# Optimization experiments

Hardware: AMD Instinct MI355X
Metric: run time of the kernel (lower is better)

The kernel has to match this reference:

```python
import jax, jax.numpy as jnp
import numpy as np

SEQ_LEN = 12
EMB = 64        # embedding_dim
H = 128         # dec_h_dim
MLP = 1024      # mlp_dim
Z = 32          # z_dim
ZX = MLP + Z    # 1056, width of cat([enc_h_feat, z])
B = 32768


def setup_inputs() -> dict:
    key = jax.random.key(0)
    ks = jax.random.split(key, 16)
    s = 0.05  # weight scale to keep the recurrence stable
    return {
        "last_pos": jax.random.normal(ks[0], (B, 2), jnp.float32),
        "last_pos_rel": jax.random.normal(ks[1], (B, 2), jnp.float32),
        "enc_h_feat": jax.random.normal(ks[2], (B, MLP), jnp.float32),
        "z": jax.random.normal(ks[3], (B, Z), jnp.float32),
        "seq_start_end": jnp.zeros((1, 2), jnp.int64),
        # LSTM params (PyTorch layout: gates ordered i,f,g,o along rows)
        "W_ih": jax.random.normal(ks[4], (4 * H, ZX + EMB), jnp.float32) * s,
        "W_hh": jax.random.normal(ks[5], (4 * H, H), jnp.float32) * s,
        "b_ih": jax.random.normal(ks[6], (4 * H,), jnp.float32) * s,
        "b_hh": jax.random.normal(ks[7], (4 * H,), jnp.float32) * s,
        # mlp: Linear(ZX->MLP), ReLU, Linear(MLP->H), ReLU
        "W1": jax.random.normal(ks[8], (MLP, ZX), jnp.float32) * s,
        "b1": jax.random.normal(ks[9], (MLP,), jnp.float32) * s,
        "W2": jax.random.normal(ks[10], (H, MLP), jnp.float32) * s,
        "b2": jax.random.normal(ks[11], (H,), jnp.float32) * s,
        # spatial_embedding: Linear(2 -> EMB)
        "W_sp": jax.random.normal(ks[12], (EMB, 2), jnp.float32) * s,
        "b_sp": jax.random.normal(ks[13], (EMB,), jnp.float32) * s,
        # hidden2pos: Linear(H -> 2)
        "W_hp": jax.random.normal(ks[14], (2, H), jnp.float32) * s,
        "b_hp": jax.random.normal(ks[15], (2,), jnp.float32) * s,
    }


def _decode(last_pos, last_pos_rel, enc_h_feat, z,
            W_ih, W_hh, b_ih, b_hh, W1, b1, W2, b2, W_sp, b_sp, W_hp, b_hp):
    # initial decoder input from last relative position
    dec_inp = last_pos_rel @ W_sp.T + b_sp                     # [B, EMB]
    zx = jnp.concatenate([enc_h_feat, z], axis=1)              # [B, ZX]
    h = jax.nn.relu(jax.nn.relu(zx @ W1.T + b1) @ W2.T + b2)   # [B, H]
    c = jnp.zeros_like(h)
    # zx is constant across steps: precompute its gate contribution + biases
    W_zx, W_emb = W_ih[:, :ZX], W_ih[:, ZX:]
    zx_proj = zx @ W_zx.T + b_ih + b_hh                        # [B, 4H]

    def step(carry, _):
        h, c, last_pos, dec_inp = carry
        gates = zx_proj + dec_inp @ W_emb.T + h @ W_hh.T       # [B, 4H]
        i, f, g, o = jnp.split(gates, 4, axis=1)
        c = jax.nn.sigmoid(f) * c + jax.nn.sigmoid(i) * jnp.tanh(g)
        h = jax.nn.sigmoid(o) * jnp.tanh(c)
        rel_pos = h @ W_hp.T + b_hp                            # [B, 2]
        last_pos = rel_pos + last_pos
        dec_inp = rel_pos @ W_sp.T + b_sp
        return (h, c, last_pos, dec_inp), rel_pos

    _, pred = jax.lax.scan(step, (h, c, last_pos, dec_inp), None, length=SEQ_LEN)
    return pred  # [SEQ_LEN, B, 2]


def reference(last_pos, last_pos_rel, enc_h_feat, z, seq_start_end,
              W_ih, W_hh, b_ih, b_hh, W1, b1, W2, b2, W_sp, b_sp, W_hp, b_hp):
    # seq_start_end is unused by the original forward
    return _decode(last_pos, last_pos_rel, enc_h_feat, z,
                   W_ih, W_hh, b_ih, b_hh, W1, b1, W2, b2, W_sp, b_sp, W_hp, b_hp)
```

## Files before the change

kernel.cpp:

```cpp
#include <hip/hip_runtime.h>

#define BATCH   32768
#define SEQLEN  12
#define EMB     64
#define H       128
#define MLP     1024
#define Z       32
#define ZX      1056
#define KP      1088
#define NG      512

typedef _Float16 f16x8 __attribute__((ext_vector_type(8)));
typedef float    f32x4 __attribute__((ext_vector_type(4)));

#define S_WCAT_OFF   0u
#define S_W2H_OFF    3244032u
#define S_WHHF_OFF   3506176u
#define S_WC_OFF     3637248u
#define S_BIAS2_OFF  3641344u
#define S_T1_OFF     3643392u
#define S_GP_OFF     70752256u
#define S_H0_OFF     137861120u
#define B_WCAT_OFF   0u
#define B_W2H_OFF    3342336u
#define B_WHHF_OFF   3604480u
#define B_WC_OFF     3735552u
#define B_BIAS2_OFF  3739648u
#define B_T1_OFF     3741696u
#define B_GP_OFF     70850560u
#define B_H0_OFF     137959424u
#define B_ZX16_OFF   146348032u
#define B_TOTAL      217651200ull

__device__ __forceinline__ float sigf(float x) {
    return __builtin_amdgcn_rcpf(1.0f + __expf(-x));
}
__device__ __forceinline__ float tanhfast(float x) {
    return 2.0f * __builtin_amdgcn_rcpf(1.0f + __expf(-2.0f * x)) - 1.0f;
}

__device__ __forceinline__ void gload16(const void* g, void* l) {
    __builtin_amdgcn_global_load_lds(
        (const __attribute__((address_space(1))) unsigned int*)(unsigned long long)(uintptr_t)g,
        (__attribute__((address_space(3))) unsigned int*)(unsigned int)(uintptr_t)l,
        16, 0, 0);
}

__global__ __launch_bounds__(256) void prep_kernel(
    const float* __restrict__ W_ih, const float* __restrict__ W_hh_in,
    const float* __restrict__ b_ih, const float* __restrict__ b_hh,
    const float* __restrict__ W1,   const float* __restrict__ W2,
    const float* __restrict__ W_sp, const float* __restrict__ b_sp,
    const float* __restrict__ W_hp, int cs,
    _Float16* __restrict__ wcat, _Float16* __restrict__ w2h,
    _Float16* __restrict__ whhf, float* __restrict__ wc, float* __restrict__ bias2)
{
    const int bid = blockIdx.x;
    const int tid = threadIdx.x;
    if (bid < 1536) {
        const float* src = (bid < 1024) ? (W1 + (size_t)bid * ZX)
                                        : (W_ih + (size_t)(bid - 1024) * 1120);
        _Float16* dst = wcat + (size_t)bid * cs;
        for (int k = tid; k < cs; k += 256)
            dst[k] = (k < ZX) ? (_Float16)src[k] : (_Float16)0.f;
    } else if (bid < 1664) {
        const int n = bid - 1536;
        for (int k = tid; k < MLP; k += 256)
            w2h[n * MLP + k] = (_Float16)W2[n * MLP + k];
    } else if (bid < 1920) {
        const int n = (bid - 1664) * 2 + (tid >> 7);
        const int k = tid & 127;
        float wc0 = 0.f, wc1 = 0.f;
        for (int e = 0; e < EMB; ++e) {
            const float we = W_ih[(size_t)n * 1120 + ZX + e];
            wc0 += we * W_sp[e * 2];
            wc1 += we * W_sp[e * 2 + 1];
        }
        whhf[n * H + k] = (_Float16)(W_hh_in[n * H + k] + wc0 * W_hp[k] + wc1 * W_hp[H + k]);
    } else {
        const int t = (bid - 1920) * 256 + tid;
        if (t < 1024) {
            const int n = t >> 1, j = t & 1;
            float s = 0.f;
            for (int e = 0; e < EMB; ++e)
                s += W_ih[(size_t)n * 1120 + ZX + e] * W_sp[e * 2 + j];
            wc[t] = s;
        } else if (t < 1536) {
            const int n = t - 1024;
            float s = b_ih[n] + b_hh[n];
            for (int e = 0; e < EMB; ++e)
                s += W_ih[(size_t)n * 1120 + ZX + e] * b_sp[e];
            bias2[n] = s;
        }
    }
}

__global__ __launch_bounds__(256) void zxcast_kernel(
    const float* __restrict__ enc, const float* __restrict__ zin,
    _Float16* __restrict__ zx16)
{
    const int gid = blockIdx.x * 256 + threadIdx.x;
    if (gid < 4194304) {
        const int row = gid >> 7, cw = gid & 127;
        const float4* s = (const float4*)(enc + (size_t)row * MLP + cw * 8);
        const float4 f0 = s[0], f1 = s[1];
        f16x8 v = {(_Float16)f0.x, (_Float16)f0.y, (_Float16)f0.z, (_Float16)f0.w,
                   (_Float16)f1.x, (_Float16)f1.y, (_Float16)f1.z, (_Float16)f1.w};
        *(f16x8*)(zx16 + (size_t)row * KP + cw * 8) = v;
    } else if (gid < 4325376) {
        const int g2 = gid - 4194304;
        const int row = g2 >> 2, cw = g2 & 3;
        const float4* s = (const float4*)(zin + (size_t)row * Z + cw * 8);
        const float4 f0 = s[0], f1 = s[1];
        f16x8 v = {(_Float16)f0.x, (_Float16)f0.y, (_Float16)f0.z, (_Float16)f0.w,
                   (_Float16)f1.x, (_Float16)f1.y, (_Float16)f1.z, (_Float16)f1.w};
        *(f16x8*)(zx16 + (size_t)row * KP + MLP + cw * 8) = v;
    } else {
        const int g2 = gid - 4325376;
        const int row = g2 >> 2, cw = g2 & 3;
        f16x8 v = {};
        *(f16x8*)(zx16 + (size_t)row * KP + ZX + cw * 8) = v;
    }
}

__global__ __launch_bounds__(512, 2) void gemm1_big_kernel(
    const _Float16* __restrict__ zx16, const _Float16* __restrict__ wcat,
    const float* __restrict__ bias1, const float* __restrict__ bias2g,
    _Float16* __restrict__ t1, float* __restrict__ gperm)
{
    __shared__ _Float16 s_a[2][256 * 64];
    __shared__ _Float16 s_b[2][256 * 64];

    const int tid = threadIdx.x;
    const int b   = blockIdx.x;
    const int swz = (b & 7) * 96 + (b >> 3);
    const int mt  = swz / 6, nt = swz % 6;
    const int m0  = mt * 256, n0 = nt * 256;

    const int lane = tid & 63, wv = tid >> 6;
    const int wm   = wv >> 2,  wn = wv & 3;
    const int l15  = lane & 15, q = lane >> 4;

    const int rowS = tid >> 3;
    const int chS  = (tid & 7) ^ (rowS & 7);

    const _Float16* gA = zx16 + (size_t)(m0 + rowS) * KP + chS * 8;
    const _Float16* gB = wcat + (size_t)(n0 + rowS) * KP + chS * 8;
    const size_t rstep = (size_t)64 * KP;

    const int ph0  = q ^ (l15 & 7);
    const int ph1  = (4 + q) ^ (l15 & 7);
    const int aof0 = (wm * 128 + l15) * 64 + ph0 * 8;
    const int aof1 = (wm * 128 + l15) * 64 + ph1 * 8;
    const int bof0 = (wn * 64 + l15) * 64 + ph0 * 8;
    const int bof1 = (wn * 64 + l15) * 64 + ph1 * 8;

    f32x4 acc[8][4] = {};

    {
        _Float16* dA = &s_a[0][0] + wv * 512;
        _Float16* dB = &s_b[0][0] + wv * 512;
        #pragma unroll
        for (int j = 0; j < 4; ++j) gload16(gA + j * rstep, dA + j * 4096);
        #pragma unroll
        for (int j = 0; j < 4; ++j) gload16(gB + j * rstep, dB + j * 4096);
    }

    #pragma unroll 2
    for (int kt = 0; kt < 16; ++kt) {
        const int cur = kt & 1;
        const _Float16* sA = &s_a[cur][0];
        const _Float16* sB = &s_b[cur][0];
        _Float16* dA = &s_a[cur ^ 1][0] + wv * 512;
        _Float16* dB = &s_b[cur ^ 1][0] + wv * 512;
        const _Float16* gA1 = gA + (kt + 1) * 64;
        const _Float16* gB1 = gB + (kt + 1) * 64;

        f16x8 af[4], bf[4];

        gload16(gA1,         dA);
        gload16(gA1 + rstep, dA + 4096);
        asm volatile("s_waitcnt vmcnt(2)\n\ts_barrier" ::: "memory");
        #pragma unroll
        for (int i = 0; i < 4; ++i) af[i] = *(const f16x8*)(sA + aof0 + i * 1024);
        #pragma unroll
        for (int i = 0; i < 4; ++i) bf[i] = *(const f16x8*)(sB + bof0 + i * 1024);
        __builtin_amdgcn_s_setprio(1);
        #pragma unroll
        for (int n_ = 0; n_ < 4; ++n_)
            #pragma unroll
            for (int m_ = 0; m_ < 4; ++m_)
                acc[m_][n_] = __builtin_amdgcn_mfma_f32_16x16x32_f16(af[m_], bf[n_], acc[m_][n_], 0, 0, 0);
        __builtin_amdgcn_s_setprio(0);
        asm volatile("s_barrier" ::: "memory");

        gload16(gA1 + 2 * rstep, dA + 8192);
        gload16(gA1 + 3 * rstep, dA + 12288);
        #pragma unroll
        for (int i = 0; i < 4; ++i) af[i] = *(const f16x8*)(sA + aof0 + 4096 + i * 1024);
        asm volatile("s_barrier" ::: "memory");
        __builtin_amdgcn_s_setprio(1);
        #pragma unroll
        for (int n_ = 0; n_ < 4; ++n_)
            #pragma unroll
            for (int m_ = 0; m_ < 4; ++m_)
                acc[4 + m_][n_] = __builtin_amdgcn_mfma_f32_16x16x32_f16(af[m_], bf[n_], acc[4 + m_][n_], 0, 0, 0);
        __builtin_amdgcn_s_setprio(0);
        asm volatile("s_barrier" ::: "memory");

        gload16(gB1,         dB);
        gload16(gB1 + rstep, dB + 4096);
        #pragma unroll
        for (int i = 0; i < 4; ++i) af[i] = *(const f16x8*)(sA + aof1 + i * 1024);
        #pragma unroll
        for (int i = 0; i < 4; ++i) bf[i] = *(const f16x8*)(sB + bof1 + i * 1024);
        asm volatile("s_barrier" ::: "memory");
        __builtin_amdgcn_s_setprio(1);
        #pragma unroll
        for (int n_ = 0; n_ < 4; ++n_)
            #pragma unroll
            for (int m_ = 0; m_ < 4; ++m_)
                acc[m_][n_] = __builtin_amdgcn_mfma_f32_16x16x32_f16(af[m_], bf[n_], acc[m_][n_], 0, 0, 0);
        __builtin_amdgcn_s_setprio(0);
        asm volatile("s_barrier" ::: "memory");

        gload16(gB1 + 2 * rstep, dB + 8192);
        gload16(gB1 + 3 * rstep, dB + 12288);
        #pragma unroll
        for (int i = 0; i < 4; ++i) af[i] = *(const f16x8*)(sA + aof1 + 4096 + i * 1024);
        asm volatile("s_barrier" ::: "memory");
        __builtin_amdgcn_s_setprio(1);
        #pragma unroll
        for (int n_ = 0; n_ < 4; ++n_)
            #pragma unroll
            for (int m_ = 0; m_ < 4; ++m_)
                acc[4 + m_][n_] = __builtin_amdgcn_mfma_f32_16x16x32_f16(af[m_], bf[n_], acc[4 + m_][n_], 0, 0, 0);
        __builtin_amdgcn_s_setprio(0);
        asm volatile("s_barrier" ::: "memory");
    }

    {
        const _Float16* sA = &s_a[0][0];
        const _Float16* sB = &s_b[0][0];
        asm volatile("s_waitcnt vmcnt(0)\n\ts_barrier" ::: "memory");
        f16x8 af[4], bf[4];
        #pragma unroll
        for (int i = 0; i < 4; ++i) af[i] = *(const f16x8*)(sA + aof0 + i * 1024);
        #pragma unroll
        for (int i = 0; i < 4; ++i) bf[i] = *(const f16x8*)(sB + bof0 + i * 1024);
        __builtin_amdgcn_s_setprio(1);
        #pragma unroll
        for (int n_ = 0; n_ < 4; ++n_)
            #pragma unroll
            for (int m_ = 0; m_ < 4; ++m_)
                acc[m_][n_] = __builtin_amdgcn_mfma_f32_16x16x32_f16(af[m_], bf[n_], acc[m_][n_], 0, 0, 0);
        #pragma unroll
        for (int i = 0; i < 4; ++i) af[i] = *(const f16x8*)(sA + aof0 + 4096 + i * 1024);
        #pragma unroll
        for (int n_ = 0; n_ < 4; ++n_)
            #pragma unroll
            for (int m_ = 0; m_ < 4; ++m_)
                acc[4 + m_][n_] = __builtin_amdgcn_mfma_f32_16x16x32_f16(af[m_], bf[n_], acc[4 + m_][n_], 0, 0, 0);
        #pragma unroll
        for (int i = 0; i < 4; ++i) af[i] = *(const f16x8*)(sA + aof1 + i * 1024);
        #pragma unroll
        for (int i = 0; i < 4; ++i) bf[i] = *(const f16x8*)(sB + bof1 + i * 1024);
        #pragma unroll
        for (int n_ = 0; n_ < 4; ++n_)
            #pragma unroll
            for (int m_ = 0; m_ < 4; ++m_)
                acc[m_][n_] = __builtin_amdgcn_mfma_f32_16x16x32_f16(af[m_], bf[n_], acc[m_][n_], 0, 0, 0);
        #pragma unroll
        for (int i = 0; i < 4; ++i) af[i] = *(const f16x8*)(sA + aof1 + 4096 + i * 1024);
        #pragma unroll
        for (int n_ = 0; n_ < 4; ++n_)
            #pragma unroll
            for (int m_ = 0; m_ < 4; ++m_)
                acc[4 + m_][n_] = __builtin_amdgcn_mfma_f32_16x16x32_f16(af[m_], bf[n_], acc[4 + m_][n_], 0, 0, 0);
        __builtin_amdgcn_s_setprio(0);
    }

    if (nt < 4) {
        #pragma unroll
        for (int im = 0; im < 8; ++im)
            #pragma unroll
            for (int in_ = 0; in_ < 4; ++in_) {
                const int n = n0 + wn * 64 + in_ * 16 + l15;
                const float bb = bias1[n];
                const int mbase = m0 + wm * 128 + im * 16 + q * 4;
                #pragma unroll
                for (int r = 0; r < 4; ++r) {
                    float v = acc[im][in_][r] + bb;
                    v = v > 0.f ? v : 0.f;
                    t1[(size_t)(mbase + r) * MLP + n] = (_Float16)v;
                }
            }
    } else {
        #pragma unroll
        for (int im = 0; im < 8; ++im)
            #pragma unroll
            for (int in_ = 0; in_ < 4; ++in_) {
                const int n = (n0 - 1024) + wn * 64 + in_ * 16 + l15;
                const float bb = bias2g[n];
                const int m4 = (m0 + wm * 128 + im * 16 + q * 4) >> 2;
                float4 v;
                v.x = acc[im][in_][0] + bb;
                v.y = acc[im][in_][1] + bb;
                v.z = acc[im][in_][2] + bb;
                v.w = acc[im][in_][3] + bb;
                *(float4*)(gperm + ((size_t)m4 * NG + n) * 4) = v;
            }
    }
}

__global__ __launch_bounds__(256) void gemm1_small_kernel(
    const float* __restrict__ enc, const float* __restrict__ zin,
    const _Float16* __restrict__ wcat,
    const float* __restrict__ bias1, const float* __restrict__ bias2g,
    _Float16* __restrict__ t1, float* __restrict__ gperm)
{
    __shared__ float    s_a[128 * 32];
    __shared__ _Float16 s_b[128 * 32];

    const int tid = threadIdx.x;
    const int b = blockIdx.x;
    const int x = b & 7, s = b >> 3;
    const int mt = x * 32 + s / 12;
    const int bn = s % 12;
    const int m0 = mt * 128;

    const int lane = tid & 63, wv = tid >> 6;
    const int wm = wv >> 1, wn = wv & 1;
    const int l15 = lane & 15, q = lane >> 4;

    const int rowA = tid >> 3;
    const int chA  = (tid & 7) ^ ((tid >> 3) & 7);
    const int rowB = tid >> 2;
    const int chB  = (tid & 3) ^ ((tid >> 3) & 3);

    const int ca0 = (2 * q) ^ (l15 & 7);
    const int cb  = q ^ ((l15 >> 1) & 3);

    f32x4 acc[4][4] = {};

    for (int kt = 0; kt < 33; ++kt) {
        const float* abase;
        size_t astride;
        if (kt < 32) { abase = enc + (size_t)m0 * MLP + kt * 32; astride = MLP; }
        else         { abase = zin + (size_t)m0 * Z;             astride = Z;   }

        __syncthreads();
        #pragma unroll
        for (int i = 0; i < 4; ++i)
            gload16(abase + (size_t)(i * 32 + rowA) * astride + chA * 4,
                    s_a + i * 1024 + wv * 256);
        #pragma unroll
        for (int i = 0; i < 2; ++i)
            gload16(wcat + (size_t)(bn * 128 + i * 64 + rowB) * ZX + kt * 32 + chB * 8,
                    s_b + i * 2048 + wv * 512);
        __syncthreads();

        f16x8 af[4];
        #pragma unroll
        for (int im = 0; im < 4; ++im) {
            const float* ap = s_a + (wm * 64 + im * 16 + l15) * 32;
            const float4 f0 = *(const float4*)(ap + ca0 * 4);
            const float4 f1 = *(const float4*)(ap + (ca0 ^ 1) * 4);
            af[im] = f16x8{(_Float16)f0.x, (_Float16)f0.y, (_Float16)f0.z, (_Float16)f0.w,
                           (_Float16)f1.x, (_Float16)f1.y, (_Float16)f1.z, (_Float16)f1.w};
        }
        #pragma unroll
        for (int in_ = 0; in_ < 4; ++in_) {
            const f16x8 bf = *(const f16x8*)(s_b + (wn * 64 + in_ * 16 + l15) * 32 + cb * 8);
            #pragma unroll
            for (int im = 0; im < 4; ++im)
                acc[im][in_] = __builtin_amdgcn_mfma_f32_16x16x32_f16(af[im], bf, acc[im][in_], 0, 0, 0);
        }
    }

    if (bn < 8) {
        #pragma unroll
        for (int im = 0; im < 4; ++im)
            #pragma unroll
            for (int in_ = 0; in_ < 4; ++in_) {
                const int n = bn * 128 + wn * 64 + in_ * 16 + l15;
                const float bb = bias1[n];
                #pragma unroll
                for (int r = 0; r < 4; ++r) {
                    const int m = m0 + wm * 64 + im * 16 + q * 4 + r;
                    float v = acc[im][in_][r] + bb;
                    v = v > 0.f ? v : 0.f;
                    t1[(size_t)m * MLP + n] = (_Float16)v;
                }
            }
    } else {
        #pragma unroll
        for (int im = 0; im < 4; ++im)
            #pragma unroll
            for (int in_ = 0; in_ < 4; ++in_) {
                const int n = (bn - 8) * 128 + wn * 64 + in_ * 16 + l15;
                const float bb = bias2g[n];
                const int m4 = (m0 + wm * 64 + im * 16 + q * 4) >> 2;
                float4 v;
                v.x = acc[im][in_][0] + bb;
                v.y = acc[im][in_][1] + bb;
                v.z = acc[im][in_][2] + bb;
                v.w = acc[im][in_][3] + bb;
                *(float4*)(gperm + ((size_t)m4 * NG + n) * 4) = v;
            }
    }
}

__global__ __launch_bounds__(256) void gemm2_kernel(
    const _Float16* __restrict__ t1, const _Float16* __restrict__ w2h,
    const float* __restrict__ b2, _Float16* __restrict__ h0buf)
{
    __shared__ _Float16 s_a[2][64 * 32];
    __shared__ _Float16 s_b[2][128 * 32];

    const int tid = threadIdx.x;
    const int m0  = blockIdx.x * 64;
    const int lane = tid & 63, wv = tid >> 6;
    const int l15 = lane & 15, q = lane >> 4;

    const int rowS = tid >> 2;
    const int chS  = ((tid & 3) ^ (tid >> 2) ^ (tid >> 4)) & 3;
    const int phF  = (q ^ l15 ^ (l15 >> 2)) & 3;

    const int rowB0 = rowS, rowB1 = 64 + rowS;
    const int cB0 = ((tid & 3) ^ rowB0 ^ (rowB0 >> 2)) & 3;
    const int cB1 = ((tid & 3) ^ rowB1 ^ (rowB1 >> 2)) & 3;

    const _Float16* gA  = t1  + (size_t)(m0 + rowS) * MLP + chS * 8;
    const _Float16* gB0 = w2h + (size_t)rowB0 * MLP + cB0 * 8;
    const _Float16* gB1 = w2h + (size_t)rowB1 * MLP + cB1 * 8;

    f32x4 acc[4][2] = {};

    gload16(gA,  &s_a[0][0] + wv * 512);
    gload16(gB0, &s_b[0][0] + wv * 512);
    gload16(gB1, &s_b[0][0] + 2048 + wv * 512);

    for (int kt = 0; kt < 32; ++kt) {
        const int cur = kt & 1;
        if (kt < 31) {
            const int nxt = cur ^ 1;
            gload16(gA  + (kt + 1) * 32, &s_a[nxt][0] + wv * 512);
            gload16(gB0 + (kt + 1) * 32, &s_b[nxt][0] + wv * 512);
            gload16(gB1 + (kt + 1) * 32, &s_b[nxt][0] + 2048 + wv * 512);
            asm volatile("s_waitcnt vmcnt(3)\n\ts_barrier" ::: "memory");
        } else {
            asm volatile("s_waitcnt vmcnt(0)\n\ts_barrier" ::: "memory");
        }

        f16x8 af[4];
        #pragma unroll
        for (int im = 0; im < 4; ++im)
            af[im] = *(const f16x8*)(&s_a[cur][0] + (im * 16 + l15) * 32 + phF * 8);
        #pragma unroll
        for (int in_ = 0; in_ < 2; ++in_) {
            const f16x8 bf = *(const f16x8*)(&s_b[cur][0] + (wv * 32 + in_ * 16 + l15) * 32 + phF * 8);
            #pragma unroll
            for (int im = 0; im < 4; ++im)
                acc[im][in_] = __builtin_amdgcn_mfma_f32_16x16x32_f16(af[im], bf, acc[im][in_], 0, 0, 0);
        }
        asm volatile("s_barrier" ::: "memory");
    }

    #pragma unroll
    for (int im = 0; im < 4; ++im)
        #pragma unroll
        for (int in_ = 0; in_ < 2; ++in_) {
            const int n = wv * 32 + in_ * 16 + l15;
            const float bb = b2[n];
            #pragma unroll
            for (int r = 0; r < 4; ++r) {
                const int m = m0 + im * 16 + q * 4 + r;
                float v = acc[im][in_][r] + bb;
                v = v > 0.f ? v : 0.f;
                h0buf[(size_t)m * H + n] = (_Float16)v;
            }
        }
}

__global__ __launch_bounds__(512) void recur_kernel(
    const float* __restrict__ gperm, const _Float16* __restrict__ h0buf,
    const _Float16* __restrict__ whhf, const float* __restrict__ wc,
    const float* __restrict__ whp, const float* __restrict__ bhp,
    const float* __restrict__ lpr, float* __restrict__ out)
{
    __shared__ _Float16 s_whh[512 * 136];
    __shared__ _Float16 s_h[64 * 136];
    __shared__ float    s_p[128];
    __shared__ float    s_wc[1024];
    __shared__ float    s_whp[256];
    __shared__ float    s_bhp[2];

    const int tid = threadIdx.x;
    const int m0  = blockIdx.x * 64;
    const int lane = tid & 63, w = tid >> 6;
    const int l15 = lane & 15, q = lane >> 4;

    #pragma unroll
    for (int i = 0; i < 16; ++i) {
        const int cid = tid + i * 512;
        const int row = cid >> 4, ch = cid & 15;
        *(uint4*)(s_whh + row * 136 + ch * 8) = *(const uint4*)(whhf + row * H + ch * 8);
    }
    if (tid < 256) *(float4*)(s_wc + tid * 4)  = *(const float4*)(wc + tid * 4);
    if (tid < 64)  *(float4*)(s_whp + tid * 4) = *(const float4*)(whp + tid * 4);
    if (tid < 2)   s_bhp[tid] = bhp[tid];
    if (tid < 128) s_p[tid] = lpr[(size_t)m0 * 2 + tid];
    {
        const int row = tid >> 3, ch = tid & 7;
        *(uint4*)(s_h + row * 136 + ch * 16)     = *(const uint4*)(h0buf + (size_t)(m0 + row) * H + ch * 16);
        *(uint4*)(s_h + row * 136 + ch * 16 + 8) = *(const uint4*)(h0buf + (size_t)(m0 + row) * H + ch * 16 + 8);
    }

    f32x4 gb[4][4];
    #pragma unroll
    for (int im = 0; im < 4; ++im) {
        const int m4 = (m0 >> 2) + im * 4 + q;
        #pragma unroll
        for (int g = 0; g < 4; ++g) {
            const float4 v = *(const float4*)(gperm + ((size_t)m4 * NG + g * H + w * 16 + l15) * 4);
            gb[im][g] = f32x4{v.x, v.y, v.z, v.w};
        }
    }

    f32x4 cst[4] = {};

    __syncthreads();

    {
        const int part = tid & 3;
        const int j    = (tid >> 2) & 1;
        const int row  = tid >> 3;
        float sum = 0.f;
        #pragma unroll
        for (int u = 0; u < 4; ++u) {
            const f16x8 hv = *(const f16x8*)(s_h + row * 136 + part * 32 + u * 8);
            const float4* wp = (const float4*)(s_whp + j * H + part * 32 + u * 8);
            const float4 w0 = wp[0], w1 = wp[1];
            sum += (float)hv[0] * w0.x + (float)hv[1] * w0.y + (float)hv[2] * w0.z + (float)hv[3] * w0.w
                 + (float)hv[4] * w1.x + (float)hv[5] * w1.y + (float)hv[6] * w1.z + (float)hv[7] * w1.w;
        }
        sum += __shfl_down(sum, 2, 64);
        sum += __shfl_down(sum, 1, 64);
        if (part == 0) s_p[row * 2 + j] -= sum;
    }
    __syncthreads();

    float wc0[4], wc1[4], cg[4];
    #pragma unroll
    for (int g = 0; g < 4; ++g) {
        const int n = g * H + w * 16 + l15;
        wc0[g] = s_wc[n * 2];
        wc1[g] = s_wc[n * 2 + 1];
        cg[g]  = wc0[g] * s_bhp[0] + wc1[g] * s_bhp[1];
    }
    #pragma unroll
    for (int im = 0; im < 4; ++im)
        #pragma unroll
        for (int r = 0; r < 4; ++r) {
            const int mrow = im * 16 + q * 4 + r;
            const float pa = s_p[mrow * 2], pb = s_p[mrow * 2 + 1];
            #pragma unroll
            for (int g = 0; g < 4; ++g)
                gb[im][g][r] += pa * wc0[g] + pb * wc1[g];
        }

    for (int t = 0; t < SEQLEN; ++t) {
        f32x4 acc[4][4];
        #pragma unroll
        for (int kt = 0; kt < 4; ++kt) {
            f16x8 af[4];
            #pragma unroll
            for (int im = 0; im < 4; ++im)
                af[im] = *(const f16x8*)(s_h + (im * 16 + l15) * 136 + kt * 32 + q * 8);
            #pragma unroll
            for (int g = 0; g < 4; ++g) {
                const f16x8 bf = *(const f16x8*)(s_whh + (g * H + w * 16 + l15) * 136 + kt * 32 + q * 8);
                #pragma unroll
                for (int im = 0; im < 4; ++im)
                    acc[im][g] = __builtin_amdgcn_mfma_f32_16x16x32_f16(
                        af[im], bf, (kt == 0) ? gb[im][g] : acc[im][g], 0, 0, 0);
            }
        }
        __syncthreads();

        #pragma unroll
        for (int im = 0; im < 4; ++im) {
            #pragma unroll
            for (int r = 0; r < 4; ++r) {
                const int mrow = im * 16 + q * 4 + r;
                const float cc = sigf(acc[im][1][r]) * cst[im][r]
                               + sigf(acc[im][0][r]) * tanhfast(acc[im][2][r]);
                cst[im][r] = cc;
                const float hh = sigf(acc[im][3][r]) * tanhfast(cc);
                s_h[mrow * 136 + w * 16 + l15] = (_Float16)hh;
            }
        }
        if (t == 0) {
            #pragma unroll
            for (int im = 0; im < 4; ++im)
                #pragma unroll
                for (int r = 0; r < 4; ++r) {
                    const int mrow = im * 16 + q * 4 + r;
                    const float pa = s_p[mrow * 2], pb = s_p[mrow * 2 + 1];
                    #pragma unroll
                    for (int g = 0; g < 4; ++g)
                        gb[im][g][r] += cg[g] - (pa * wc0[g] + pb * wc1[g]);
                }
        }
        __syncthreads();

        {
            const int part = tid & 3;
            const int j    = (tid >> 2) & 1;
            const int row  = tid >> 3;
            float sum = 0.f;
            #pragma unroll
            for (int u = 0; u < 4; ++u) {
                const f16x8 hv = *(const f16x8*)(s_h + row * 136 + part * 32 + u * 8);
                const float4* wp = (const float4*)(s_whp + j * H + part * 32 + u * 8);
                const float4 w0 = wp[0], w1 = wp[1];
                sum += (float)hv[0] * w0.x + (float)hv[1] * w0.y + (float)hv[2] * w0.z + (float)hv[3] * w0.w
                     + (float)hv[4] * w1.x + (float)hv[5] * w1.y + (float)hv[6] * w1.z + (float)hv[7] * w1.w;
            }
            sum += __shfl_down(sum, 2, 64);
            sum += __shfl_down(sum, 1, 64);
            if (part == 0)
                out[(size_t)t * (BATCH * 2) + (size_t)(m0 + row) * 2 + j] = sum + s_bhp[j];
        }
    }
}

extern "C" void kernel_launch(void* const* d_in, const int* in_sizes, int n_in,
                              void* d_out, int out_size, void* d_ws, size_t ws_size,
                              hipStream_t stream)
{
    const float* last_pos_rel = (const float*)d_in[1];
    const float* enc          = (const float*)d_in[2];
    const float* zin          = (const float*)d_in[3];
    const float* W_ih         = (const float*)d_in[5];
    const float* W_hh         = (const float*)d_in[6];
    const float* b_ih         = (const float*)d_in[7];
    const float* b_hh         = (const float*)d_in[8];
    const float* W1           = (const float*)d_in[9];
    const float* b1           = (const float*)d_in[10];
    const float* W2           = (const float*)d_in[11];
    const float* b2           = (const float*)d_in[12];
    const float* W_sp         = (const float*)d_in[13];
    const float* b_sp         = (const float*)d_in[14];
    const float* W_hp         = (const float*)d_in[15];
    const float* b_hp         = (const float*)d_in[16];
    float* out = (float*)d_out;

    char* ws = (char*)d_ws;
    const bool big = (ws_size >= B_TOTAL);

    _Float16* wcat  = (_Float16*)(ws + (big ? B_WCAT_OFF  : S_WCAT_OFF));
    _Float16* w2h   = (_Float16*)(ws + (big ? B_W2H_OFF   : S_W2H_OFF));
    _Float16* whhf  = (_Float16*)(ws + (big ? B_WHHF_OFF  : S_WHHF_OFF));
    float*    wc    = (float*)(ws + (big ? B_WC_OFF    : S_WC_OFF));
    float*    bias2 = (float*)(ws + (big ? B_BIAS2_OFF : S_BIAS2_OFF));
    _Float16* t1    = (_Float16*)(ws + (big ? B_T1_OFF : S_T1_OFF));
    float*    gperm = (float*)(ws + (big ? B_GP_OFF : S_GP_OFF));
    _Float16* h0b   = (_Float16*)(ws + (big ? B_H0_OFF : S_H0_OFF));
    _Float16* zx16  = (_Float16*)(ws + B_ZX16_OFF);

    prep_kernel<<<dim3(1926), 256, 0, stream>>>(W_ih, W_hh, b_ih, b_hh, W1, W2, W_sp, b_sp,
                                                W_hp, big ? KP : ZX, wcat, w2h, whhf, wc, bias2);
    if (big) {
        zxcast_kernel<<<dim3(17408), 256, 0, stream>>>(enc, zin, zx16);
        gemm1_big_kernel<<<dim3(768), 512, 0, stream>>>(zx16, wcat, b1, bias2, t1, gperm);
    } else {
        gemm1_small_kernel<<<dim3(3072), 256, 0, stream>>>(enc, zin, wcat, b1, bias2, t1, gperm);
    }
    gemm2_kernel<<<dim3(512), 256, 0, stream>>>(t1, w2h, b2, h0b);
    recur_kernel<<<dim3(512), 512, 0, stream>>>(gperm, h0b, whhf, wc, W_hp, b_hp,
                                                last_pos_rel, out);
}
```

Measured before the change: 483.7 us.

## Merge weight prep with zx cast kernel and simplify GEMM1 k-loop pipeline

Result: no change. 488.0 us (+0.9%).

```diff
diff --git a/kernel.cpp b/kernel.cpp
--- a/kernel.cpp
+++ b/kernel.cpp
@@ -46,60 +46,60 @@
         16, 0, 0);
 }
 
-__global__ __launch_bounds__(256) void prep_kernel(
+__global__ __launch_bounds__(256) void prepzx_kernel(
     const float* __restrict__ W_ih, const float* __restrict__ W_hh_in,
     const float* __restrict__ b_ih, const float* __restrict__ b_hh,
     const float* __restrict__ W1,   const float* __restrict__ W2,
     const float* __restrict__ W_sp, const float* __restrict__ b_sp,
     const float* __restrict__ W_hp, int cs,
     _Float16* __restrict__ wcat, _Float16* __restrict__ w2h,
-    _Float16* __restrict__ whhf, float* __restrict__ wc, float* __restrict__ bias2)
-{
-    const int bid = blockIdx.x;
-    const int tid = threadIdx.x;
-    if (bid < 1536) {
-        const float* src = (bid < 1024) ? (W1 + (size_t)bid * ZX)
-                                        : (W_ih + (size_t)(bid - 1024) * 1120);
-        _Float16* dst = wcat + (size_t)bid * cs;
-        for (int k = tid; k < cs; k += 256)
-            dst[k] = (k < ZX) ? (_Float16)src[k] : (_Float16)0.f;
-    } else if (bid < 1664) {
-        const int n = bid - 1536;
-        for (int k = tid; k < MLP; k += 256)
-            w2h[n * MLP + k] = (_Float16)W2[n * MLP + k];
-    } else if (bid < 1920) {
-        const int n = (bid - 1664) * 2 + (tid >> 7);
-        const int k = tid & 127;
-        float wc0 = 0.f, wc1 = 0.f;
-        for (int e = 0; e < EMB; ++e) {
-            const float we = W_ih[(size_t)n * 1120 + ZX + e];
-            wc0 += we * W_sp[e * 2];
-            wc1 += we * W_sp[e * 2 + 1];
-        }
-        whhf[n * H + k] = (_Float16)(W_hh_in[n * H + k] + wc0 * W_hp[k] + wc1 * W_hp[H + k]);
-    } else {
-        const int t = (bid - 1920) * 256 + tid;
-        if (t < 1024) {
-            const int n = t >> 1, j = t & 1;
-            float s = 0.f;
-            for (int e = 0; e < EMB; ++e)
-                s += W_ih[(size_t)n * 1120 + ZX + e] * W_sp[e * 2 + j];
-            wc[t] = s;
-        } else if (t < 1536) {
-            const int n = t - 1024;
-            float s = b_ih[n] + b_hh[n];
-            for (int e = 0; e < EMB; ++e)
-                s += W_ih[(size_t)n * 1120 + ZX + e] * b_sp[e];
-            bias2[n] = s;
-        }
-    }
-}
-
-__global__ __launch_bounds__(256) void zxcast_kernel(
+    _Float16* __restrict__ whhf, float* __restrict__ wc, float* __restrict__ bias2,
     const float* __restrict__ enc, const float* __restrict__ zin,
     _Float16* __restrict__ zx16)
 {
-    const int gid = blockIdx.x * 256 + threadIdx.x;
+    const int tid = threadIdx.x;
+    if (blockIdx.x < 1926u) {
+        const int bid = blockIdx.x;
+        if (bid < 1536) {
+            const float* src = (bid < 1024) ? (W1 + (size_t)bid * ZX)
+                                            : (W_ih + (size_t)(bid - 1024) * 1120);
+            _Float16* dst = wcat + (size_t)bid * cs;
+            for (int k = tid; k < cs; k += 256)
+                dst[k] = (k < ZX) ? (_Float16)src[k] : (_Float16)0.f;
+        } else if (bid < 1664) {
+            const int n = bid - 1536;
+            for (int k = tid; k < MLP; k += 256)
+                w2h[n * MLP + k] = (_Float16)W2[n * MLP + k];
+        } else if (bid < 1920) {
+            const int n = (bid - 1664) * 2 + (tid >> 7);
+            const int k = tid & 127;
+            float wc0 = 0.f, wc1 = 0.f;
+            for (int e = 0; e < EMB; ++e) {
+                const float we = W_ih[(size_t)n * 1120 + ZX + e];
+                wc0 += we * W_sp[e * 2];
+                wc1 += we * W_sp[e * 2 + 1];
+            }
+            whhf[n * H + k] = (_Float16)(W_hh_in[n * H + k] + wc0 * W_hp[k] + wc1 * W_hp[H + k]);
+        } else {
+            const int t = (bid - 1920) * 256 + tid;
+            if (t < 1024) {
+                const int n = t >> 1, j = t & 1;
+                float s = 0.f;
+                for (int e = 0; e < EMB; ++e)
+                    s += W_ih[(size_t)n * 1120 + ZX + e] * W_sp[e * 2 + j];
+                wc[t] = s;
+            } else if (t < 1536) {
+                const int n = t - 1024;
+                float s = b_ih[n] + b_hh[n];
+                for (int e = 0; e < EMB; ++e)
+                    s += W_ih[(size_t)n * 1120 + ZX + e] * b_sp[e];
+                bias2[n] = s;
+            }
+        }
+        return;
+    }
+
+    const int gid = (blockIdx.x - 1926) * 256 + tid;
     if (gid < 4194304) {
         const int row = gid >> 7, cw = gid & 127;
         const float4* s = (const float4*)(enc + (size_t)row * MLP + cw * 8);
@@ -176,60 +176,41 @@
         const _Float16* gA1 = gA + (kt + 1) * 64;
         const _Float16* gB1 = gB + (kt + 1) * 64;
 
+        #pragma unroll
+        for (int j = 0; j < 4; ++j) gload16(gA1 + j * rstep, dA + j * 4096);
+        #pragma unroll
+        for (int j = 0; j < 4; ++j) gload16(gB1 + j * rstep, dB + j * 4096);
+        asm volatile("s_waitcnt vmcnt(8)\n\ts_barrier" ::: "memory");
+
         f16x8 af[4], bf[4];
-
-        gload16(gA1,         dA);
-        gload16(gA1 + rstep, dA + 4096);
-        asm volatile("s_waitcnt vmcnt(2)\n\ts_barrier" ::: "memory");
+        __builtin_amdgcn_s_setprio(1);
         #pragma unroll
         for (int i = 0; i < 4; ++i) af[i] = *(const f16x8*)(sA + aof0 + i * 1024);
         #pragma unroll
         for (int i = 0; i < 4; ++i) bf[i] = *(const f16x8*)(sB + bof0 + i * 1024);
-        __builtin_amdgcn_s_setprio(1);
         #pragma unroll
         for (int n_ = 0; n_ < 4; ++n_)
             #pragma unroll
             for (int m_ = 0; m_ < 4; ++m_)
                 acc[m_][n_] = __builtin_amdgcn_mfma_f32_16x16x32_f16(af[m_], bf[n_], acc[m_][n_], 0, 0, 0);
-        __builtin_amdgcn_s_setprio(0);
-        asm volatile("s_barrier" ::: "memory");
-
-        gload16(gA1 + 2 * rstep, dA + 8192);
-        gload16(gA1 + 3 * rstep, dA + 12288);
         #pragma unroll
         for (int i = 0; i < 4; ++i) af[i] = *(const f16x8*)(sA + aof0 + 4096 + i * 1024);
-        asm volatile("s_barrier" ::: "memory");
-        __builtin_amdgcn_s_setprio(1);
         #pragma unroll
         for (int n_ = 0; n_ < 4; ++n_)
             #pragma unroll
             for (int m_ = 0; m_ < 4; ++m_)
                 acc[4 + m_][n_] = __builtin_amdgcn_mfma_f32_16x16x32_f16(af[m_], bf[n_], acc[4 + m_][n_], 0, 0, 0);
-        __builtin_amdgcn_s_setprio(0);
-        asm volatile("s_barrier" ::: "memory");
-
-        gload16(gB1,         dB);
-        gload16(gB1 + rstep, dB + 4096);
         #pragma unroll
         for (int i = 0; i < 4; ++i) af[i] = *(const f16x8*)(sA + aof1 + i * 1024);
         #pragma unroll
         for (int i = 0; i < 4; ++i) bf[i] = *(const f16x8*)(sB + bof1 + i * 1024);
-        asm volatile("s_barrier" ::: "memory");
-        __builtin_amdgcn_s_setprio(1);
         #pragma unroll
         for (int n_ = 0; n_ < 4; ++n_)
             #pragma unroll
             for (int m_ = 0; m_ < 4; ++m_)
                 acc[m_][n_] = __builtin_amdgcn_mfma_f32_16x16x32_f16(af[m_], bf[n_], acc[m_][n_], 0, 0, 0);
-        __builtin_amdgcn_s_setprio(0);
-        asm volatile("s_barrier" ::: "memory");
-
-        gload16(gB1 + 2 * rstep, dB + 8192);
-        gload16(gB1 + 3 * rstep, dB + 12288);
         #pragma unroll
         for (int i = 0; i < 4; ++i) af[i] = *(const f16x8*)(sA + aof1 + 4096 + i * 1024);
-        asm volatile("s_barrier" ::: "memory");
-        __builtin_amdgcn_s_setprio(1);
         #pragma unroll
         for (int n_ = 0; n_ < 4; ++n_)
             #pragma unroll
@@ -244,11 +225,11 @@
         const _Float16* sB = &s_b[0][0];
         asm volatile("s_waitcnt vmcnt(0)\n\ts_barrier" ::: "memory");
         f16x8 af[4], bf[4];
+        __builtin_amdgcn_s_setprio(1);
         #pragma unroll
         for (int i = 0; i < 4; ++i) af[i] = *(const f16x8*)(sA + aof0 + i * 1024);
         #pragma unroll
         for (int i = 0; i < 4; ++i) bf[i] = *(const f16x8*)(sB + bof0 + i * 1024);
-        __builtin_amdgcn_s_setprio(1);
         #pragma unroll
         for (int n_ = 0; n_ < 4; ++n_)
             #pragma unroll
@@ -670,10 +651,11 @@
     _Float16* h0b   = (_Float16*)(ws + (big ? B_H0_OFF : S_H0_OFF));
     _Float16* zx16  = (_Float16*)(ws + B_ZX16_OFF);
 
-    prep_kernel<<<dim3(1926), 256, 0, stream>>>(W_ih, W_hh, b_ih, b_hh, W1, W2, W_sp, b_sp,
-                                                W_hp, big ? KP : ZX, wcat, w2h, whhf, wc, bias2);
+    const int nzx = big ? 17408 : 0;
+    prepzx_kernel<<<dim3(1926 + nzx), 256, 0, stream>>>(
+        W_ih, W_hh, b_ih, b_hh, W1, W2, W_sp, b_sp, W_hp, big ? KP : ZX,
+        wcat, w2h, whhf, wc, bias2, enc, zin, zx16);
     if (big) {
-        zxcast_kernel<<<dim3(17408), 256, 0, stream>>>(enc, zin, zx16);
         gemm1_big_kernel<<<dim3(768), 512, 0, stream>>>(zx16, wcat, b1, bias2, t1, gperm);
     } else {
         gemm1_small_kernel<<<dim3(3072), 256, 0, stream>>>(enc, zin, wcat, b1, bias2, t1, gperm);
```
